# Kernel tuning notes

Measured on AMD Instinct MI355X. Metric: run time of the kernel, lower is better.

## Reference

```python
import jax, jax.numpy as jnp
import numpy as np

DT = 0.01  # continuous-time step for the S4D/Vandermonde reservoir kernel


def setup_inputs() -> dict:
    key = jax.random.key(0)
    ks = jax.random.split(key, 10)
    B, H, L, N = 16, 128, 4096, 64
    u = jax.random.normal(ks[0], (B, H, L), dtype=jnp.float32)
    # stable diagonal SSM: real part of Lambda strictly negative
    lambda_re = -0.5 * jax.random.uniform(ks[1], (H, N), dtype=jnp.float32) - 0.1
    lambda_im = jax.random.normal(ks[2], (H, N), dtype=jnp.float32) * np.pi
    w_re = jax.random.normal(ks[3], (H, N), dtype=jnp.float32) / np.sqrt(N)
    w_im = jax.random.normal(ks[4], (H, N), dtype=jnp.float32) / np.sqrt(N)
    d = jax.random.normal(ks[5], (H,), dtype=jnp.float32)
    mlp_w1 = jax.random.normal(ks[6], (H, H), dtype=jnp.float32) / np.sqrt(H)
    mlp_b1 = jnp.zeros((H,), dtype=jnp.float32)
    mlp_w2 = jax.random.normal(ks[7], (H, H), dtype=jnp.float32) / np.sqrt(H)
    mlp_b2 = jnp.zeros((H,), dtype=jnp.float32)
    return {"u": u, "lambda_re": lambda_re, "lambda_im": lambda_im,
            "w_re": w_re, "w_im": w_im, "d": d,
            "mlp_w1": mlp_w1, "mlp_b1": mlp_b1,
            "mlp_w2": mlp_w2, "mlp_b2": mlp_b2}


def reference(u, lambda_re, lambda_im, w_re, w_im, d,
              mlp_w1, mlp_b1, mlp_w2, mlp_b2):
    B, H, L = u.shape
    Lam = lambda_re + 1j * lambda_im          # (H, N) diagonal state matrix
    W = w_re + 1j * w_im                      # (H, N) merged C*B readout
    ell = jnp.arange(L, dtype=jnp.float32)
    # Vandermonde kernel: K[h, l] = sum_n W[h,n] * exp(dt * Lambda[h,n] * l)
    V = jnp.exp((DT * Lam)[:, :, None] * ell[None, None, :])  # (H, N, L)
    K = jnp.einsum('hn,hnl->hl', W, V)                         # (H, L) complex
    # causal FFT convolution (pad to 2L to avoid circular wrap)
    n = 2 * L
    y = jnp.fft.ifft(jnp.fft.fft(u, n=n, axis=-1) * jnp.fft.fft(K, n=n, axis=-1)[None],
                     n=n, axis=-1)[..., :L]
    y = y + d[None, :, None] * u              # skip / feed-through term
    y = y.real                                # Real() projection
    # 1x1-conv MLP with ReLU (mlp_layers = 2)
    h1 = jax.nn.relu(jnp.einsum('oh,bhl->bol', mlp_w1, y) + mlp_b1[None, :, None])
    y2 = jax.nn.relu(jnp.einsum('oh,bhl->bol', mlp_w2, h1) + mlp_b2[None, :, None])
    return y2
```

## Files before the change

kernel.cpp:

```cpp
#include <hip/hip_runtime.h>
#include <hip/hip_bf16.h>

#define B_ 16
#define H_ 128
#define L_ 4096
#define N_ 64
#define DT_ 0.01f

typedef __bf16 bf16;
typedef __bf16 bf16x8 __attribute__((ext_vector_type(8)));
typedef __bf16 bf16x4 __attribute__((ext_vector_type(4)));
typedef float f32x4 __attribute__((ext_vector_type(4)));

#define USWZ(c, k) ((c) * 64 + (((((k) >> 4) ^ ((c) & 3)) << 4) | ((k) & 15)))
#define SSWZ(c, k) ((c) * 128 + (((((k) >> 4) ^ ((c) & 7)) << 4) | ((k) & 15)))

__global__ __launch_bounds__(512, 4) void k_ssm3(
        const float* __restrict__ u,
        const float* __restrict__ lre, const float* __restrict__ lim,
        const float* __restrict__ wre, const float* __restrict__ wim,
        const float* __restrict__ dv,
        const float* __restrict__ w1, const float* __restrict__ w2,
        bf16* __restrict__ w1b, bf16* __restrict__ w2b,
        bf16* __restrict__ ybf) {
    alignas(16) __shared__ char smem[68352];
    bf16*  Ubf  = (bf16*)smem;
    float* Ctr  = (float*)(smem + 8192);
    bf16*  Sbf  = (bf16*)(smem + 41472);
    bf16*  Tm   = (bf16*)(smem + 57856);
    float* lamS = (float*)(smem + 67072);
    float* taps = (float*)(smem + 68096);

    const int tid  = threadIdx.x;
    const int lane = tid & 63, wv = tid >> 6;
    const int cl   = lane & 15, q = lane >> 4;
    const int bId  = blockIdx.x;
    const int h    = bId & 127;
    const int bg   = bId >> 7;

    if (tid < 64) {
        if (bId < 256) w1b[bId * 64 + tid] = (bf16)w1[bId * 64 + tid];
        else           w2b[(bId - 256) * 64 + tid] = (bf16)w2[(bId - 256) * 64 + tid];
    }
    if (tid < 64) {
        lamS[tid]       = lre[h * 64 + tid] * DT_;
        lamS[64 + tid]  = lim[h * 64 + tid] * DT_;
        lamS[128 + tid] = wre[h * 64 + tid];
        lamS[192 + tid] = wim[h * 64 + tid];
    }
    __syncthreads();

    bf16x8 pA0, pA1;
    {
        const int row = wv * 16 + cl;
        const int n = row & 63;
        const bool isIm = row >= 64;
        const float lr = lamS[n], li = lamS[64 + n];
        #pragma unroll
        for (int jj = 0; jj < 8; ++jj) {
            const float p0 = (float)(63 - (q * 8 + jj));
            const float e0 = __expf(p0 * lr);
            pA0[jj] = (bf16)(isIm ? e0 * __sinf(p0 * li) : e0 * __cosf(p0 * li));
            const float p1 = (float)(63 - (32 + q * 8 + jj));
            const float e1 = __expf(p1 * lr);
            pA1[jj] = (bf16)(isIm ? e1 * __sinf(p1 * li) : e1 * __cosf(p1 * li));
        }
    }
    bf16x8 qA[4];
    {
        const float fd = (float)((wv >> 1) * 16 + cl + 1);
        #pragma unroll
        for (int ks = 0; ks < 4; ++ks) {
            #pragma unroll
            for (int nn = 0; nn < 4; ++nn) {
                const int n = ks * 16 + q * 4 + nn;
                const float lr = lamS[n], li = lamS[64 + n];
                const float wr = lamS[128 + n], wi = lamS[192 + n];
                const float e  = __expf(fd * lr);
                const float cr = e * __cosf(fd * li), ci = e * __sinf(fd * li);
                qA[ks][2 * nn]     = (bf16)(wr * cr - wi * ci);
                qA[ks][2 * nn + 1] = (bf16)(-(wr * ci + wi * cr));
            }
        }
    }
    float a64r, a64i;
    {
        const float lr = lamS[lane], li = lamS[64 + lane];
        const float e = __expf(64.f * lr);
        a64r = e * __cosf(64.f * li);
        a64i = e * __sinf(64.f * li);
    }
    {
        const float lr = lamS[lane], li = lamS[64 + lane];
        const float wr = lamS[128 + lane], wi = lamS[192 + lane];
        #pragma unroll
        for (int i = 0; i < 8; ++i) {
            const int dlt = wv * 8 + i;
            const float fd = (float)dlt;
            const float e = __expf(fd * lr);
            float t = wr * e * __cosf(fd * li) - wi * e * __sinf(fd * li);
            #pragma unroll
            for (int d = 1; d < 64; d <<= 1) t += __shfl_xor(t, d, 64);
            if (lane == 0) taps[dlt] = t;
        }
    }
    __syncthreads();

    {
        const int dlt = tid >> 3, j0 = (tid & 7) << 3;
        const float dh = dv[h];
        bf16x8 t;
        #pragma unroll
        for (int e = 0; e < 8; ++e) {
            const int j = j0 + e;
            float v = (j <= dlt) ? taps[dlt - j] : 0.f;
            if (j == dlt) v += dh;
            t[e] = (bf16)v;
        }
        *(bf16x8*)(&Tm[dlt * 72 + j0]) = t;
    }

    const int mt = wv >> 1, nt0 = (wv & 1) * 2;
    for (int it = 0; it < 4; ++it) {
        const int bh = (bg * 4 + it) * 128 + h;
        const float* __restrict__ up = u + (size_t)bh * L_;

        {
            const int c = tid >> 3, j0 = (tid & 7) << 3;
            const float4* src = (const float4*)(up + c * 64 + j0);
            const float4 f0 = src[0], f1 = src[1];
            bf16x8 t;
            t[0] = (bf16)f0.x; t[1] = (bf16)f0.y; t[2] = (bf16)f0.z; t[3] = (bf16)f0.w;
            t[4] = (bf16)f1.x; t[5] = (bf16)f1.y; t[6] = (bf16)f1.z; t[7] = (bf16)f1.w;
            *(bf16x8*)(&Ubf[USWZ(c, j0)]) = t;
        }
        __syncthreads();

        {
            f32x4 acc[4];
            #pragma unroll
            for (int nt = 0; nt < 4; ++nt) acc[nt] = (f32x4){0.f, 0.f, 0.f, 0.f};
            #pragma unroll
            for (int nt = 0; nt < 4; ++nt) {
                const int c = nt * 16 + cl;
                const bf16x8 b0 = *(const bf16x8*)(&Ubf[USWZ(c, q * 8)]);
                acc[nt] = __builtin_amdgcn_mfma_f32_16x16x32_bf16(pA0, b0, acc[nt], 0, 0, 0);
                const bf16x8 bq = *(const bf16x8*)(&Ubf[USWZ(c, 32 + q * 8)]);
                acc[nt] = __builtin_amdgcn_mfma_f32_16x16x32_bf16(pA1, bq, acc[nt], 0, 0, 0);
            }
            #pragma unroll
            for (int nt = 0; nt < 4; ++nt)
                #pragma unroll
                for (int r = 0; r < 4; ++r)
                    Ctr[(wv * 16 + q * 4 + r) * 65 + nt * 16 + cl] = acc[nt][r];
        }
        __syncthreads();

        f32x4 acc2[2];
        acc2[0] = (f32x4){0.f, 0.f, 0.f, 0.f};
        acc2[1] = (f32x4){0.f, 0.f, 0.f, 0.f};
        if (wv == 0) {
            float sr = 0.f, si = 0.f;
            #pragma unroll 8
            for (int c = 0; c < 64; ++c) {
                bf16* sp = &Sbf[SSWZ(c, 2 * lane)];
                sp[0] = (bf16)sr;
                sp[1] = (bf16)si;
                const float cr = Ctr[lane * 65 + c];
                const float ci = Ctr[(64 + lane) * 65 + c];
                const float nr = fmaf(a64r, sr, fmaf(-a64i, si, cr));
                const float ni = fmaf(a64r, si, fmaf(a64i, sr, ci));
                sr = nr; si = ni;
            }
        } else {
            #pragma unroll
            for (int ks = 0; ks < 2; ++ks) {
                const int k0 = ks * 32 + q * 8;
                const bf16x8 a = *(const bf16x8*)(&Tm[(mt * 16 + cl) * 72 + k0]);
                #pragma unroll
                for (int j = 0; j < 2; ++j) {
                    const int c = (nt0 + j) * 16 + cl;
                    const bf16x8 bfr = *(const bf16x8*)(&Ubf[USWZ(c, k0)]);
                    acc2[j] = __builtin_amdgcn_mfma_f32_16x16x32_bf16(a, bfr, acc2[j], 0, 0, 0);
                }
            }
        }
        __syncthreads();

        if (wv == 0) {
            #pragma unroll
            for (int ks = 0; ks < 2; ++ks) {
                const int k0 = ks * 32 + q * 8;
                const bf16x8 a = *(const bf16x8*)(&Tm[(mt * 16 + cl) * 72 + k0]);
                #pragma unroll
                for (int j = 0; j < 2; ++j) {
                    const int c = (nt0 + j) * 16 + cl;
                    const bf16x8 bfr = *(const bf16x8*)(&Ubf[USWZ(c, k0)]);
                    acc2[j] = __builtin_amdgcn_mfma_f32_16x16x32_bf16(a, bfr, acc2[j], 0, 0, 0);
                }
            }
        }
        {
            #pragma unroll
            for (int ks = 0; ks < 4; ++ks) {
                const int k0 = ks * 32 + q * 8;
                #pragma unroll
                for (int j = 0; j < 2; ++j) {
                    const int c = (nt0 + j) * 16 + cl;
                    const bf16x8 bfr = *(const bf16x8*)(&Sbf[SSWZ(c, k0)]);
                    acc2[j] = __builtin_amdgcn_mfma_f32_16x16x32_bf16(qA[ks], bfr, acc2[j], 0, 0, 0);
                }
            }
            bf16* Yb = (bf16*)Ctr;
            #pragma unroll
            for (int j = 0; j < 2; ++j) {
                const int c = (nt0 + j) * 16 + cl;
                bf16x4 yv;
                #pragma unroll
                for (int r = 0; r < 4; ++r) yv[r] = (bf16)acc2[j][r];
                *(bf16x4*)(&Yb[c * 72 + mt * 16 + q * 4]) = yv;
            }
        }
        __syncthreads();

        {
            const bf16* Yb = (const bf16*)Ctr;
            const int c = tid >> 3, s0 = (tid & 7) << 3;
            const bf16x8 v = *(const bf16x8*)(&Yb[c * 72 + s0]);
            *(bf16x8*)(ybf + (size_t)bh * L_ + c * 64 + s0) = v;
        }
        __syncthreads();
    }
}

#define YSTR 136
__global__ __launch_bounds__(256, 6) void k_mlp(
        const bf16* __restrict__ ybf,
        const bf16* __restrict__ w1b, const bf16* __restrict__ w2b,
        const float* __restrict__ b1, const float* __restrict__ b2,
        float* __restrict__ out) {
    __shared__ bf16 YT[64 * YSTR];
    __shared__ float B1s[H_], B2s[H_];

    const int tid = threadIdx.x;
    const int b   = blockIdx.x >> 6;
    const int lt  = blockIdx.x & 63;
    const int l0  = lt * 64;

    if (tid < H_) { B1s[tid] = b1[tid]; B2s[tid] = b2[tid]; }

    {
        const int h  = tid >> 1;
        const int lh = (tid & 1) * 32;
        const bf16x8* src = (const bf16x8*)(ybf + ((size_t)b * H_ + h) * L_ + l0 + lh);
        #pragma unroll
        for (int v = 0; v < 4; ++v) {
            bf16x8 d = src[v];
            #pragma unroll
            for (int e = 0; e < 8; ++e) YT[(lh + v * 8 + e) * YSTR + h] = d[e];
        }
    }
    __syncthreads();

    const int lane = tid & 63;
    const int wv   = tid >> 6;
    const int m    = lane & 15;
    const int q    = lane >> 4;
    const int m0   = wv * 32;

    f32x4 acc[2][4];
    #pragma unroll
    for (int i = 0; i < 2; ++i)
        #pragma unroll
        for (int nt = 0; nt < 4; ++nt) acc[i][nt] = (f32x4){0.f, 0.f, 0.f, 0.f};

    #pragma unroll
    for (int kb = 0; kb < 4; ++kb) {
        const bf16x8 a0 = *(const bf16x8*)(w1b + (size_t)(m0 + m)      * H_ + kb * 32 + q * 8);
        const bf16x8 a1 = *(const bf16x8*)(w1b + (size_t)(m0 + 16 + m) * H_ + kb * 32 + q * 8);
        #pragma unroll
        for (int nt = 0; nt < 4; ++nt) {
            const bf16x8 bfr = *(const bf16x8*)(&YT[(nt * 16 + m) * YSTR + kb * 32 + q * 8]);
            acc[0][nt] = __builtin_amdgcn_mfma_f32_16x16x32_bf16(a0, bfr, acc[0][nt], 0, 0, 0);
            acc[1][nt] = __builtin_amdgcn_mfma_f32_16x16x32_bf16(a1, bfr, acc[1][nt], 0, 0, 0);
        }
    }
    __syncthreads();

    #pragma unroll
    for (int i = 0; i < 2; ++i) {
        const int o0 = m0 + 16 * i + 4 * q;
        #pragma unroll
        for (int nt = 0; nt < 4; ++nt) {
            const f32x4 v = acc[i][nt];
            bf16x4 hv;
            #pragma unroll
            for (int r = 0; r < 4; ++r) {
                float x = v[r] + B1s[o0 + r];
                hv[r] = (bf16)fmaxf(x, 0.f);
            }
            *(bf16x4*)(&YT[(nt * 16 + m) * YSTR + o0]) = hv;
        }
    }
    __syncthreads();

    f32x4 acc2[2][4];
    #pragma unroll
    for (int i = 0; i < 2; ++i)
        #pragma unroll
        for (int nt = 0; nt < 4; ++nt) acc2[i][nt] = (f32x4){0.f, 0.f, 0.f, 0.f};

    #pragma unroll
    for (int kb = 0; kb < 4; ++kb) {
        const bf16x8 a0 = *(const bf16x8*)(w2b + (size_t)(m0 + m)      * H_ + kb * 32 + q * 8);
        const bf16x8 a1 = *(const bf16x8*)(w2b + (size_t)(m0 + 16 + m) * H_ + kb * 32 + q * 8);
        #pragma unroll
        for (int nt = 0; nt < 4; ++nt) {
            const bf16x8 bfr = *(const bf16x8*)(&YT[(nt * 16 + m) * YSTR + kb * 32 + q * 8]);
            acc2[0][nt] = __builtin_amdgcn_mfma_f32_16x16x32_bf16(a0, bfr, acc2[0][nt], 0, 0, 0);
            acc2[1][nt] = __builtin_amdgcn_mfma_f32_16x16x32_bf16(a1, bfr, acc2[1][nt], 0, 0, 0);
        }
    }

    #pragma unroll
    for (int i = 0; i < 2; ++i) {
        const int o0 = m0 + 16 * i + 4 * q;
        #pragma unroll
        for (int nt = 0; nt < 4; ++nt) {
            const f32x4 v = acc2[i][nt];
            #pragma unroll
            for (int r = 0; r < 4; ++r) {
                float x = v[r] + B2s[o0 + r];
                x = fmaxf(x, 0.f);
                out[((size_t)b * H_ + o0 + r) * L_ + l0 + nt * 16 + m] = x;
            }
        }
    }
}

extern "C" void kernel_launch(void* const* d_in, const int* in_sizes, int n_in,
                              void* d_out, int out_size, void* d_ws, size_t ws_size,
                              hipStream_t stream) {
    const float* u   = (const float*)d_in[0];
    const float* lre = (const float*)d_in[1];
    const float* lim = (const float*)d_in[2];
    const float* wre = (const float*)d_in[3];
    const float* wim = (const float*)d_in[4];
    const float* dv  = (const float*)d_in[5];
    const float* w1  = (const float*)d_in[6];
    const float* b1  = (const float*)d_in[7];
    const float* w2  = (const float*)d_in[8];
    const float* b2  = (const float*)d_in[9];
    float* out = (float*)d_out;

    char* ws = (char*)d_ws;
    bf16* ybf = (bf16*)ws;   ws += (size_t)B_ * H_ * L_ * 2;
    bf16* w1b = (bf16*)ws;   ws += H_ * H_ * 2;
    bf16* w2b = (bf16*)ws;   ws += H_ * H_ * 2;

    hipLaunchKernelGGL(k_ssm3, dim3(512), dim3(512), 0, stream,
                       u, lre, lim, wre, wim, dv, w1, w2, w1b, w2b, ybf);
    hipLaunchKernelGGL(k_mlp, dim3(B_ * (L_ / 64)), dim3(256), 0, stream,
                       ybf, w1b, w2b, b1, b2, out);
}
```

Measured before the change: 129.3 us.

## Parallelize chunk-state recurrence with shuffle scan, prefetch next u tile, pack transpose

```diff
diff --git a/kernel.cpp b/kernel.cpp
--- a/kernel.cpp
+++ b/kernel.cpp
@@ -10,6 +10,7 @@
 typedef __bf16 bf16;
 typedef __bf16 bf16x8 __attribute__((ext_vector_type(8)));
 typedef __bf16 bf16x4 __attribute__((ext_vector_type(4)));
+typedef __bf16 bf16x2 __attribute__((ext_vector_type(2)));
 typedef float f32x4 __attribute__((ext_vector_type(4)));
 
 #define USWZ(c, k) ((c) * 64 + (((((k) >> 4) ^ ((c) & 3)) << 4) | ((k) & 15)))
@@ -37,12 +38,14 @@
     const int bId  = blockIdx.x;
     const int h    = bId & 127;
     const int bg   = bId >> 7;
+    const int c0   = tid >> 3, j0 = (tid & 7) << 3;
+
+    const float4* ps0 = (const float4*)(u + (size_t)((bg * 4) * 128 + h) * L_ + c0 * 64 + j0);
+    const float4 f0 = ps0[0], f1 = ps0[1];
 
     if (tid < 64) {
         if (bId < 256) w1b[bId * 64 + tid] = (bf16)w1[bId * 64 + tid];
         else           w2b[(bId - 256) * 64 + tid] = (bf16)w2[(bId - 256) * 64 + tid];
-    }
-    if (tid < 64) {
         lamS[tid]       = lre[h * 64 + tid] * DT_;
         lamS[64 + tid]  = lim[h * 64 + tid] * DT_;
         lamS[128 + tid] = wre[h * 64 + tid];
@@ -83,12 +86,14 @@
             }
         }
     }
-    float a64r, a64i;
-    {
-        const float lr = lamS[lane], li = lamS[64 + lane];
+    float a64r[8], a64i[8];
+    #pragma unroll
+    for (int m = 0; m < 8; ++m) {
+        const int n = wv * 8 + m;
+        const float lr = lamS[n], li = lamS[64 + n];
         const float e = __expf(64.f * lr);
-        a64r = e * __cosf(64.f * li);
-        a64i = e * __sinf(64.f * li);
+        a64r[m] = e * __cosf(64.f * li);
+        a64i[m] = e * __sinf(64.f * li);
     }
     {
         const float lr = lamS[lane], li = lamS[64 + lane];
@@ -104,37 +109,39 @@
             if (lane == 0) taps[dlt] = t;
         }
     }
-    __syncthreads();
-
-    {
-        const int dlt = tid >> 3, j0 = (tid & 7) << 3;
+    {
+        bf16x8 t;
+        t[0] = (bf16)f0.x; t[1] = (bf16)f0.y; t[2] = (bf16)f0.z; t[3] = (bf16)f0.w;
+        t[4] = (bf16)f1.x; t[5] = (bf16)f1.y; t[6] = (bf16)f1.z; t[7] = (bf16)f1.w;
+        *(bf16x8*)(&Ubf[USWZ(c0, j0)]) = t;
+    }
+    __syncthreads();
+
+    {
+        const int dlt = tid >> 3, jj0 = (tid & 7) << 3;
         const float dh = dv[h];
         bf16x8 t;
         #pragma unroll
         for (int e = 0; e < 8; ++e) {
-            const int j = j0 + e;
+            const int j = jj0 + e;
             float v = (j <= dlt) ? taps[dlt - j] : 0.f;
             if (j == dlt) v += dh;
             t[e] = (bf16)v;
         }
-        *(bf16x8*)(&Tm[dlt * 72 + j0]) = t;
+        *(bf16x8*)(&Tm[dlt * 72 + jj0]) = t;
     }
 
     const int mt = wv >> 1, nt0 = (wv & 1) * 2;
+    float4 pf0, pf1;
     for (int it = 0; it < 4; ++it) {
         const int bh = (bg * 4 + it) * 128 + h;
-        const float* __restrict__ up = u + (size_t)bh * L_;
-
-        {
-            const int c = tid >> 3, j0 = (tid & 7) << 3;
-            const float4* src = (const float4*)(up + c * 64 + j0);
-            const float4 f0 = src[0], f1 = src[1];
-            bf16x8 t;
-            t[0] = (bf16)f0.x; t[1] = (bf16)f0.y; t[2] = (bf16)f0.z; t[3] = (bf16)f0.w;
-            t[4] = (bf16)f1.x; t[5] = (bf16)f1.y; t[6] = (bf16)f1.z; t[7] = (bf16)f1.w;
-            *(bf16x8*)(&Ubf[USWZ(c, j0)]) = t;
-        }
-        __syncthreads();
+
+        {
+            const int itn = it < 3 ? it + 1 : 3;
+            const float4* ps = (const float4*)(u + (size_t)((bg * 4 + itn) * 128 + h) * L_
+                                               + c0 * 64 + j0);
+            pf0 = ps[0]; pf1 = ps[1];
+        }
 
         {
             f32x4 acc[4];
@@ -156,61 +163,64 @@
         }
         __syncthreads();
 
+        {
+            float cre[8], cim[8];
+            #pragma unroll
+            for (int m = 0; m < 8; ++m) {
+                const int n = wv * 8 + m;
+                cre[m] = Ctr[n * 65 + lane];
+                cim[m] = Ctr[(64 + n) * 65 + lane];
+            }
+            #pragma unroll
+            for (int m = 0; m < 8; ++m) {
+                float ar = a64r[m], ai = a64i[m];
+                float sr = cre[m], si = cim[m];
+                #pragma unroll
+                for (int d = 1; d < 64; d <<= 1) {
+                    float tr = __shfl_up(sr, d, 64);
+                    float ti = __shfl_up(si, d, 64);
+                    if (lane < d) { tr = 0.f; ti = 0.f; }
+                    sr = fmaf(ar, tr, fmaf(-ai, ti, sr));
+                    si = fmaf(ar, ti, fmaf(ai, tr, si));
+                    const float nr = fmaf(ar, ar, -(ai * ai));
+                    ai = 2.f * ar * ai;
+                    ar = nr;
+                }
+                float xr = __shfl_up(sr, 1, 64);
+                float xi = __shfl_up(si, 1, 64);
+                if (lane == 0) { xr = 0.f; xi = 0.f; }
+                bf16* sp = &Sbf[SSWZ(lane, 2 * (wv * 8 + m))];
+                sp[0] = (bf16)xr;
+                sp[1] = (bf16)xi;
+            }
+        }
+        __syncthreads();
+
         f32x4 acc2[2];
         acc2[0] = (f32x4){0.f, 0.f, 0.f, 0.f};
         acc2[1] = (f32x4){0.f, 0.f, 0.f, 0.f};
-        if (wv == 0) {
-            float sr = 0.f, si = 0.f;
-            #pragma unroll 8
-            for (int c = 0; c < 64; ++c) {
-                bf16* sp = &Sbf[SSWZ(c, 2 * lane)];
-                sp[0] = (bf16)sr;
-                sp[1] = (bf16)si;
-                const float cr = Ctr[lane * 65 + c];
-                const float ci = Ctr[(64 + lane) * 65 + c];
-                const float nr = fmaf(a64r, sr, fmaf(-a64i, si, cr));
-                const float ni = fmaf(a64r, si, fmaf(a64i, sr, ci));
-                sr = nr; si = ni;
-            }
-        } else {
-            #pragma unroll
-            for (int ks = 0; ks < 2; ++ks) {
-                const int k0 = ks * 32 + q * 8;
-                const bf16x8 a = *(const bf16x8*)(&Tm[(mt * 16 + cl) * 72 + k0]);
-                #pragma unroll
-                for (int j = 0; j < 2; ++j) {
-                    const int c = (nt0 + j) * 16 + cl;
-                    const bf16x8 bfr = *(const bf16x8*)(&Ubf[USWZ(c, k0)]);
-                    acc2[j] = __builtin_amdgcn_mfma_f32_16x16x32_bf16(a, bfr, acc2[j], 0, 0, 0);
-                }
-            }
-        }
-        __syncthreads();
-
-        if (wv == 0) {
-            #pragma unroll
-            for (int ks = 0; ks < 2; ++ks) {
-                const int k0 = ks * 32 + q * 8;
-                const bf16x8 a = *(const bf16x8*)(&Tm[(mt * 16 + cl) * 72 + k0]);
-                #pragma unroll
-                for (int j = 0; j < 2; ++j) {
-                    const int c = (nt0 + j) * 16 + cl;
-                    const bf16x8 bfr = *(const bf16x8*)(&Ubf[USWZ(c, k0)]);
-                    acc2[j] = __builtin_amdgcn_mfma_f32_16x16x32_bf16(a, bfr, acc2[j], 0, 0, 0);
-                }
-            }
-        }
-        {
-            #pragma unroll
-            for (int ks = 0; ks < 4; ++ks) {
-                const int k0 = ks * 32 + q * 8;
-                #pragma unroll
-                for (int j = 0; j < 2; ++j) {
-                    const int c = (nt0 + j) * 16 + cl;
-                    const bf16x8 bfr = *(const bf16x8*)(&Sbf[SSWZ(c, k0)]);
-                    acc2[j] = __builtin_amdgcn_mfma_f32_16x16x32_bf16(qA[ks], bfr, acc2[j], 0, 0, 0);
-                }
-            }
+        #pragma unroll
+        for (int ks = 0; ks < 2; ++ks) {
+            const int k0 = ks * 32 + q * 8;
+            const bf16x8 a = *(const bf16x8*)(&Tm[(mt * 16 + cl) * 72 + k0]);
+            #pragma unroll
+            for (int j = 0; j < 2; ++j) {
+                const int c = (nt0 + j) * 16 + cl;
+                const bf16x8 bfr = *(const bf16x8*)(&Ubf[USWZ(c, k0)]);
+                acc2[j] = __builtin_amdgcn_mfma_f32_16x16x32_bf16(a, bfr, acc2[j], 0, 0, 0);
+            }
+        }
+        #pragma unroll
+        for (int ks = 0; ks < 4; ++ks) {
+            const int k0 = ks * 32 + q * 8;
+            #pragma unroll
+            for (int j = 0; j < 2; ++j) {
+                const int c = (nt0 + j) * 16 + cl;
+                const bf16x8 bfr = *(const bf16x8*)(&Sbf[SSWZ(c, k0)]);
+                acc2[j] = __builtin_amdgcn_mfma_f32_16x16x32_bf16(qA[ks], bfr, acc2[j], 0, 0, 0);
+            }
+        }
+        {
             bf16* Yb = (bf16*)Ctr;
             #pragma unroll
             for (int j = 0; j < 2; ++j) {
@@ -225,9 +235,14 @@
 
         {
             const bf16* Yb = (const bf16*)Ctr;
-            const int c = tid >> 3, s0 = (tid & 7) << 3;
-            const bf16x8 v = *(const bf16x8*)(&Yb[c * 72 + s0]);
-            *(bf16x8*)(ybf + (size_t)bh * L_ + c * 64 + s0) = v;
+            const bf16x8 v = *(const bf16x8*)(&Yb[c0 * 72 + j0]);
+            *(bf16x8*)(ybf + (size_t)bh * L_ + c0 * 64 + j0) = v;
+        }
+        if (it < 3) {
+            bf16x8 t;
+            t[0] = (bf16)pf0.x; t[1] = (bf16)pf0.y; t[2] = (bf16)pf0.z; t[3] = (bf16)pf0.w;
+            t[4] = (bf16)pf1.x; t[5] = (bf16)pf1.y; t[6] = (bf16)pf1.z; t[7] = (bf16)pf1.w;
+            *(bf16x8*)(&Ubf[USWZ(c0, j0)]) = t;
         }
         __syncthreads();
     }
@@ -250,14 +265,16 @@
     if (tid < H_) { B1s[tid] = b1[tid]; B2s[tid] = b2[tid]; }
 
     {
-        const int h  = tid >> 1;
-        const int lh = (tid & 1) * 32;
-        const bf16x8* src = (const bf16x8*)(ybf + ((size_t)b * H_ + h) * L_ + l0 + lh);
-        #pragma unroll
-        for (int v = 0; v < 4; ++v) {
-            bf16x8 d = src[v];
-            #pragma unroll
-            for (int e = 0; e < 8; ++e) YT[(lh + v * 8 + e) * YSTR + h] = d[e];
+        const int h0  = (tid & 63) * 2;
+        const int lh  = (tid >> 6) * 16;
+        const bf16x8* s0 = (const bf16x8*)(ybf + ((size_t)b * H_ + h0)     * L_ + l0 + lh);
+        const bf16x8* s1 = (const bf16x8*)(ybf + ((size_t)b * H_ + h0 + 1) * L_ + l0 + lh);
+        const bf16x8 r00 = s0[0], r01 = s0[1];
+        const bf16x8 r10 = s1[0], r11 = s1[1];
+        #pragma unroll
+        for (int e = 0; e < 8; ++e) {
+            *(bf16x2*)(&YT[(lh + e)     * YSTR + h0]) = (bf16x2){r00[e], r10[e]};
+            *(bf16x2*)(&YT[(lh + 8 + e) * YSTR + h0]) = (bf16x2){r01[e], r11[e]};
         }
     }
     __syncthreads();
```

Result: slower. 167.8 us (+29.8%).

## Prefetch next u tile across iterations and pair bf16 stores in MLP transpose

Applied to the files above, without the earlier changes.

```diff
diff --git a/kernel.cpp b/kernel.cpp
--- a/kernel.cpp
+++ b/kernel.cpp
@@ -10,6 +10,7 @@
 typedef __bf16 bf16;
 typedef __bf16 bf16x8 __attribute__((ext_vector_type(8)));
 typedef __bf16 bf16x4 __attribute__((ext_vector_type(4)));
+typedef __bf16 bf16x2 __attribute__((ext_vector_type(2)));
 typedef float f32x4 __attribute__((ext_vector_type(4)));
 
 #define USWZ(c, k) ((c) * 64 + (((((k) >> 4) ^ ((c) & 3)) << 4) | ((k) & 15)))
@@ -37,12 +38,14 @@
     const int bId  = blockIdx.x;
     const int h    = bId & 127;
     const int bg   = bId >> 7;
+    const int c0   = tid >> 3, j0 = (tid & 7) << 3;
+
+    const float4* ps0 = (const float4*)(u + (size_t)((bg * 4) * 128 + h) * L_ + c0 * 64 + j0);
+    const float4 f0 = ps0[0], f1 = ps0[1];
 
     if (tid < 64) {
         if (bId < 256) w1b[bId * 64 + tid] = (bf16)w1[bId * 64 + tid];
         else           w2b[(bId - 256) * 64 + tid] = (bf16)w2[(bId - 256) * 64 + tid];
-    }
-    if (tid < 64) {
         lamS[tid]       = lre[h * 64 + tid] * DT_;
         lamS[64 + tid]  = lim[h * 64 + tid] * DT_;
         lamS[128 + tid] = wre[h * 64 + tid];
@@ -104,37 +107,32 @@
             if (lane == 0) taps[dlt] = t;
         }
     }
-    __syncthreads();
-
-    {
-        const int dlt = tid >> 3, j0 = (tid & 7) << 3;
+    {
+        bf16x8 t;
+        t[0] = (bf16)f0.x; t[1] = (bf16)f0.y; t[2] = (bf16)f0.z; t[3] = (bf16)f0.w;
+        t[4] = (bf16)f1.x; t[5] = (bf16)f1.y; t[6] = (bf16)f1.z; t[7] = (bf16)f1.w;
+        *(bf16x8*)(&Ubf[USWZ(c0, j0)]) = t;
+    }
+    __syncthreads();
+
+    {
+        const int dlt = tid >> 3, jj0 = (tid & 7) << 3;
         const float dh = dv[h];
         bf16x8 t;
         #pragma unroll
         for (int e = 0; e < 8; ++e) {
-            const int j = j0 + e;
+            const int j = jj0 + e;
             float v = (j <= dlt) ? taps[dlt - j] : 0.f;
             if (j == dlt) v += dh;
             t[e] = (bf16)v;
         }
-        *(bf16x8*)(&Tm[dlt * 72 + j0]) = t;
+        *(bf16x8*)(&Tm[dlt * 72 + jj0]) = t;
     }
 
     const int mt = wv >> 1, nt0 = (wv & 1) * 2;
+    float4 pf0 = {0.f, 0.f, 0.f, 0.f}, pf1 = {0.f, 0.f, 0.f, 0.f};
     for (int it = 0; it < 4; ++it) {
         const int bh = (bg * 4 + it) * 128 + h;
-        const float* __restrict__ up = u + (size_t)bh * L_;
-
-        {
-            const int c = tid >> 3, j0 = (tid & 7) << 3;
-            const float4* src = (const float4*)(up + c * 64 + j0);
-            const float4 f0 = src[0], f1 = src[1];
-            bf16x8 t;
-            t[0] = (bf16)f0.x; t[1] = (bf16)f0.y; t[2] = (bf16)f0.z; t[3] = (bf16)f0.w;
-            t[4] = (bf16)f1.x; t[5] = (bf16)f1.y; t[6] = (bf16)f1.z; t[7] = (bf16)f1.w;
-            *(bf16x8*)(&Ubf[USWZ(c, j0)]) = t;
-        }
-        __syncthreads();
 
         {
             f32x4 acc[4];
@@ -155,6 +153,12 @@
                     Ctr[(wv * 16 + q * 4 + r) * 65 + nt * 16 + cl] = acc[nt][r];
         }
         __syncthreads();
+
+        if (it < 3) {
+            const float4* ps = (const float4*)(u + (size_t)((bg * 4 + it + 1) * 128 + h) * L_
+                                               + c0 * 64 + j0);
+            pf0 = ps[0]; pf1 = ps[1];
+        }
 
         f32x4 acc2[2];
         acc2[0] = (f32x4){0.f, 0.f, 0.f, 0.f};
@@ -225,9 +229,14 @@
 
         {
             const bf16* Yb = (const bf16*)Ctr;
-            const int c = tid >> 3, s0 = (tid & 7) << 3;
-            const bf16x8 v = *(const bf16x8*)(&Yb[c * 72 + s0]);
-            *(bf16x8*)(ybf + (size_t)bh * L_ + c * 64 + s0) = v;
+            const bf16x8 v = *(const bf16x8*)(&Yb[c0 * 72 + j0]);
+            *(bf16x8*)(ybf + (size_t)bh * L_ + c0 * 64 + j0) = v;
+        }
+        if (it < 3) {
+            bf16x8 t;
+            t[0] = (bf16)pf0.x; t[1] = (bf16)pf0.y; t[2] = (bf16)pf0.z; t[3] = (bf16)pf0.w;
+            t[4] = (bf16)pf1.x; t[5] = (bf16)pf1.y; t[6] = (bf16)pf1.z; t[7] = (bf16)pf1.w;
+            *(bf16x8*)(&Ubf[USWZ(c0, j0)]) = t;
         }
         __syncthreads();
     }
@@ -250,14 +259,16 @@
     if (tid < H_) { B1s[tid] = b1[tid]; B2s[tid] = b2[tid]; }
 
     {
-        const int h  = tid >> 1;
-        const int lh = (tid & 1) * 32;
-        const bf16x8* src = (const bf16x8*)(ybf + ((size_t)b * H_ + h) * L_ + l0 + lh);
-        #pragma unroll
-        for (int v = 0; v < 4; ++v) {
-            bf16x8 d = src[v];
-            #pragma unroll
-            for (int e = 0; e < 8; ++e) YT[(lh + v * 8 + e) * YSTR + h] = d[e];
+        const int h0  = (tid & 63) * 2;
+        const int lh  = (tid >> 6) * 16;
+        const bf16x8* s0 = (const bf16x8*)(ybf + ((size_t)b * H_ + h0)     * L_ + l0 + lh);
+        const bf16x8* s1 = (const bf16x8*)(ybf + ((size_t)b * H_ + h0 + 1) * L_ + l0 + lh);
+        const bf16x8 r00 = s0[0], r01 = s0[1];
+        const bf16x8 r10 = s1[0], r11 = s1[1];
+        #pragma unroll
+        for (int e = 0; e < 8; ++e) {
+            *(bf16x2*)(&YT[(lh + e)     * YSTR + h0]) = (bf16x2){r00[e], r10[e]};
+            *(bf16x2*)(&YT[(lh + 8 + e) * YSTR + h0]) = (bf16x2){r01[e], r11[e]};
         }
     }
     __syncthreads();
```

New measurement: 130.5 us. Within noise of the previous version (+1.0%).
